# Kernel optimization log

Measured on AMD Instinct MI355X. Metric: run time of the kernel, lower is better.

## Reference

```python
import jax, jax.numpy as jnp
import numpy as np

B, F_DIM, FH, FW = 2, 2048, 64, 128
C, H, W = 19, 512, 1024


def resize_bilinear_ac(x, h, w):
    # align_corners=True bilinear resize of (B, C, H, W) -> (B, C, h, w)
    Bx, Cx, Hx, Wx = x.shape
    ys = jnp.linspace(0.0, Hx - 1.0, h)
    xs = jnp.linspace(0.0, Wx - 1.0, w)
    y0 = jnp.floor(ys).astype(jnp.int32)
    y1 = jnp.minimum(y0 + 1, Hx - 1)
    wy = (ys - y0).astype(x.dtype)
    x0 = jnp.floor(xs).astype(jnp.int32)
    x1 = jnp.minimum(x0 + 1, Wx - 1)
    wx = (xs - x0).astype(x.dtype)
    r = x[:, :, y0, :] * (1 - wy)[None, None, :, None] + x[:, :, y1, :] * wy[None, None, :, None]
    return r[:, :, :, x0] * (1 - wx) + r[:, :, :, x1] * wx


def setup_inputs() -> dict:
    key = jax.random.key(0)
    k1, k2, k3, k4 = jax.random.split(key, 4)
    return {
        "source_feat": jax.random.normal(k1, (B, F_DIM, FH, FW), dtype=jnp.float32),
        "source_softmax": jax.random.uniform(k2, (B, C, H, W), dtype=jnp.float32),
        "target_feat": jax.random.normal(k3, (B, F_DIM, FH, FW), dtype=jnp.float32),
        "target_softmax": jax.random.uniform(k4, (B, C, H, W), dtype=jnp.float32),
        "norm_order": 2,
    }


def _process(feat, softmax):
    # feat: (B, F, h, w) -> (B*h*w, F); labels from bilinear-downsampled softmax argmax
    h, w = feat.shape[2], feat.shape[3]
    f2 = feat.transpose(0, 2, 3, 1).reshape(-1, feat.shape[1])
    sm_dws = resize_bilinear_ac(softmax, h, w)
    labels = jnp.argmax(sm_dws, axis=1).reshape(-1)
    return f2, labels


def _forward(source_feat, source_softmax, target_feat, target_softmax, p):
    num_class = source_softmax.shape[1]
    fdim = source_feat.shape[1]
    sf, sl = _process(source_feat, source_softmax)
    tf, tl = _process(target_feat, target_softmax)

    # mixed centroids: per-class mean over concatenated source+target pixels
    sum_s = jax.ops.segment_sum(sf, sl, num_segments=num_class)
    cnt_s = jax.ops.segment_sum(jnp.ones(sf.shape[0], sf.dtype), sl, num_segments=num_class)
    sum_t = jax.ops.segment_sum(tf, tl, num_segments=num_class)
    cnt_t = jax.ops.segment_sum(jnp.ones(tf.shape[0], tf.dtype), tl, num_segments=num_class)
    cnt = cnt_s + cnt_t
    seen = cnt > 0
    centroids = (sum_s + sum_t) / jnp.maximum(cnt, 1.0)[:, None]  # (C, F)

    inv_p = 1.0 / p

    def f_dist(f2, lab, cnt_d):
        # torch: sum_i norm(centroid_i - feat_i, p) / (n_i * F) over classes with n_i>0, / count
        dp = jnp.sum(jnp.abs(f2 - centroids[lab]) ** p, axis=1)  # (N,)
        ssq = jax.ops.segment_sum(dp, lab, num_segments=num_class)  # (C,)
        valid = cnt_d > 0
        ssq_safe = jnp.where(valid, ssq, 1.0)
        per = ssq_safe ** inv_p / (jnp.maximum(cnt_d, 1.0) * fdim)
        return jnp.sum(jnp.where(valid, per, 0.0)) / jnp.sum(valid).astype(f2.dtype)

    f_dist_source = f_dist(sf, sl, cnt_s)
    f_dist_target = f_dist(tf, tl, cnt_t)

    # intra-domain centroid-to-centroid distance over seen classes
    n_seen = jnp.sum(seen).astype(centroids.dtype)
    diffp = jnp.sum(jnp.abs(centroids[:, None, :] - centroids[None, :, :]) ** p, axis=-1)  # (C, C)
    pair_mask = seen[:, None] & seen[None, :] & (~jnp.eye(num_class, dtype=bool))
    row = jnp.sum(jnp.where(pair_mask, diffp, 0.0), axis=1)
    row_safe = jnp.where(seen, row, 1.0)
    per_i = row_safe ** inv_p / ((n_seen - 1.0) * fdim)
    c_dist = jnp.sum(jnp.where(seen, per_i, 0.0)) / n_seen

    return jnp.stack([c_dist, f_dist_source, f_dist_target])


def reference(source_feat, source_softmax, target_feat, target_softmax, norm_order):
    return _forward(source_feat, source_softmax, target_feat, target_softmax, norm_order)
```

## Files before the change

### kernel.cpp

```cpp
#include <hip/hip_runtime.h>
#include <hip/hip_bf16.h>

#define BB 2
#define FDIM 2048
#define FH 64
#define FW 128
#define NPIX (FH*FW)
#define NC 19
#define SH 512
#define SW 1024

#define KS 4
#define PXS (NPIX/KS)

#define OFF_GCNT  0
#define OFF_SQP   38912
#define OFF_SUMP  194560
#define OFF_LAB   2684928
#define OFF_CENT  2717696
#define OFF_DOTSP 2873344
#define OFF_PQP   2875168
#define OFF_CNTF  2876384
#define OFF_ROW   2876536

typedef __attribute__((ext_vector_type(8))) short short8v;
typedef __attribute__((ext_vector_type(4))) float f32x4;
typedef __attribute__((ext_vector_type(4))) float f4v;

__device__ inline short f32_to_bf16_bits(float x) {
  __hip_bfloat16 h = __float2bfloat16(x);
  return *reinterpret_cast<short*>(&h);
}
__device__ inline float bf16_bits_to_f32(short s) {
  unsigned u = ((unsigned)s & 0xFFFFu) << 16;
  return __uint_as_float(u);
}

__global__ __launch_bounds__(256) void labels_kernel(
    const float* __restrict__ sm_s, const float* __restrict__ sm_t,
    unsigned char* __restrict__ labels, unsigned int* __restrict__ gcnt) {
  __shared__ float rowbuf[2][2][512];
  __shared__ unsigned int lcnt[NC];
  int tid = threadIdx.x;
  if (tid < NC) lcnt[tid] = 0u;

  int bid = blockIdx.x;
  int xh  = bid & 1;
  int oy  = (bid >> 1) & 63;
  int b   = (bid >> 7) & 1;
  int dom = bid >> 8;

  const float* sm = dom ? sm_t : sm_s;
  const float step_y = 511.0f / 63.0f;
  const float step_x = 1023.0f / 127.0f;
  float fy = __fmul_rn((float)oy, step_y);
  int y0 = (int)floorf(fy); int y1 = min(y0 + 1, SH - 1);
  float wy = __fsub_rn(fy, (float)y0);
  float omwy = __fsub_rn(1.0f, wy);

  int ox = xh * 64 + (tid & 63);
  float fx = __fmul_rn((float)ox, step_x);
  int x0 = (int)floorf(fx); int x1 = min(x0 + 1, SW - 1);
  float wx = __fsub_rn(fx, (float)x0);
  float omwx = __fsub_rn(1.0f, wx);
  int x0l = x0 - xh * 512, x1l = x1 - xh * 512;

  const float* base = sm + (size_t)b * (NC * SH * SW);
  int r   = tid >> 7;
  int col = (tid & 127) * 4;
  size_t choff = (size_t)(r ? y1 : y0) * SW + xh * 512 + col;

  f4v regs = *(const f4v*)(base + choff);
  *(f4v*)&rowbuf[0][r][col] = regs;

  float best = -1.0f; int bestc = 127;
  for (int c = 0; c < NC; ++c) {
    if (c < NC - 1)
      regs = *(const f4v*)(base + (size_t)(c + 1) * (SH * SW) + choff);
    __syncthreads();
    if (tid < 64) {
      float v00 = rowbuf[c & 1][0][x0l];
      float v01 = rowbuf[c & 1][0][x1l];
      float v10 = rowbuf[c & 1][1][x0l];
      float v11 = rowbuf[c & 1][1][x1l];
      float r0  = __fadd_rn(__fmul_rn(v00, omwy), __fmul_rn(v10, wy));
      float r1  = __fadd_rn(__fmul_rn(v01, omwy), __fmul_rn(v11, wy));
      float val = __fadd_rn(__fmul_rn(r0, omwx), __fmul_rn(r1, wx));
      if (val > best) { best = val; bestc = c; }
    }
    if (c < NC - 1)
      *(f4v*)&rowbuf[(c + 1) & 1][r][col] = regs;
  }
  if (tid < 64) {
    int pixid = dom * 16384 + b * 8192 + oy * 128 + ox;
    labels[pixid] = (unsigned char)bestc;
    atomicAdd(&lcnt[bestc], 1u);
  }
  __syncthreads();
  if (tid < NC) gcnt[bid * NC + tid] = lcnt[tid];
}

__global__ __launch_bounds__(256, 5) void segsum_kernel(
    const float* __restrict__ feat_s, const float* __restrict__ feat_t,
    const unsigned char* __restrict__ labels,
    float* __restrict__ sump, float* __restrict__ sq_p) {
  __shared__ unsigned short Abuf[4][16][128];

  int tid = threadIdx.x;
  int wv = tid >> 6, l = tid & 63;
  int m16 = l & 15, grp = l >> 4;
  int lhalf = l >> 5;
  int lpx   = (l & 31) * 4;

  int low = blockIdx.x & 255;
  int hi  = blockIdx.x >> 8;
  int d = low >> 7, strip = low & 127;
  int b = hi & 1, ks = hi >> 1;

  const float* feat = d ? feat_t : feat_s;
  int px0 = ks * PXS + wv * 512;
  const float* fbase = feat + ((size_t)(b * FDIM + strip * 16)) * NPIX + px0;
  const unsigned char* labp = labels + (d * 2 + b) * NPIX + px0;

  unsigned short (*mybuf)[128] = Abuf[wv];

  f32x4 accS0 = {0.f,0.f,0.f,0.f}, accS1 = {0.f,0.f,0.f,0.f};
  f32x4 accQ0 = {0.f,0.f,0.f,0.f}, accQ1 = {0.f,0.f,0.f,0.f};

  f4v ld[8];

#define LOADW(W)                                                              \
  _Pragma("unroll") for (int r = 0; r < 8; ++r)                               \
    ld[r] = *(const f4v*)(fbase + (size_t)(r * 2 + lhalf) * NPIX + (W) * 128 + lpx);

#define WRITEW()                                                              \
  _Pragma("unroll") for (int r = 0; r < 8; ++r) {                             \
    int row = r * 2 + lhalf;                                                  \
    unsigned u0 = ((unsigned)(unsigned short)f32_to_bf16_bits(ld[r].x)) |     \
                  (((unsigned)(unsigned short)f32_to_bf16_bits(ld[r].y)) << 16);\
    unsigned u1 = ((unsigned)(unsigned short)f32_to_bf16_bits(ld[r].z)) |     \
                  (((unsigned)(unsigned short)f32_to_bf16_bits(ld[r].w)) << 16);\
    int wbyte = (row * 256 + (l & 31) * 8) ^ ((row & 7) << 4);                \
    *(uint2*)((char*)&mybuf[0][0] + wbyte) = make_uint2(u0, u1);              \
  }

#define COMPW(W)                                                              \
  _Pragma("unroll") for (int kt = 0; kt < 4; ++kt) {                          \
    int rbyte = (m16 * 256 + kt * 64 + grp * 16) ^ ((m16 & 7) << 4);          \
    short8v a = *(const short8v*)((const char*)&mybuf[0][0] + rbyte);         \
    short8v a2;                                                               \
    _Pragma("unroll") for (int j = 0; j < 8; ++j) {                           \
      float x = bf16_bits_to_f32(a[j]);                                       \
      a2[j] = f32_to_bf16_bits(x * x);                                        \
    }                                                                         \
    uint2 lw = *(const uint2*)(labp + (W) * 128 + kt * 32 + grp * 8);         \
    short8v b0, b1;                                                           \
    _Pragma("unroll") for (int j = 0; j < 8; ++j) {                           \
      unsigned lab = ((j < 4 ? lw.x : lw.y) >> ((j & 3) * 8)) & 0xFFu;        \
      b0[j] = (lab == (unsigned)m16)        ? (short)0x3F80 : (short)0;       \
      b1[j] = (lab == (unsigned)(m16 + 16)) ? (short)0x3F80 : (short)0;       \
    }                                                                         \
    accS0 = __builtin_amdgcn_mfma_f32_16x16x32_bf16(a,  b0, accS0, 0, 0, 0);  \
    accS1 = __builtin_amdgcn_mfma_f32_16x16x32_bf16(a,  b1, accS1, 0, 0, 0);  \
    accQ0 = __builtin_amdgcn_mfma_f32_16x16x32_bf16(a2, b0, accQ0, 0, 0, 0);  \
    accQ1 = __builtin_amdgcn_mfma_f32_16x16x32_bf16(a2, b1, accQ1, 0, 0, 0);  \
  }

  LOADW(0);
  WRITEW();

#pragma unroll
  for (int w = 0; w < 4; ++w) {
    if (w < 3) { LOADW(w + 1); }
    COMPW(w);
    if (w < 3) { WRITEW(); }
  }
#undef LOADW
#undef WRITEW
#undef COMPW

  __syncthreads();
  float* Sred = (float*)&Abuf[0][0][0];
  float* Qred = Sred + 4 * 19 * 16;

  int c0 = l & 15, frb = (l >> 4) * 4;
  *(f32x4*)&Sred[(wv * 19 + c0) * 16 + frb] = accS0;
  if (c0 < 3) *(f32x4*)&Sred[(wv * 19 + 16 + c0) * 16 + frb] = accS1;

  float q0 = accQ0[0] + accQ0[1] + accQ0[2] + accQ0[3];
  float q1 = accQ1[0] + accQ1[1] + accQ1[2] + accQ1[3];
  q0 += __shfl_xor(q0, 16, 64); q0 += __shfl_xor(q0, 32, 64);
  q1 += __shfl_xor(q1, 16, 64); q1 += __shfl_xor(q1, 32, 64);
  if (l < 16) Qred[wv * 19 + l] = q0;
  if (l < 3)  Qred[wv * 19 + 16 + l] = q1;
  __syncthreads();

  float* myslice = sump + ((size_t)(hi * 2 + d) * NC) * FDIM + strip * 16;
  for (int t = tid; t < NC * 16; t += 256) {
    int c = t >> 4, fr = t & 15;
    float sv = Sred[(0 * 19 + c) * 16 + fr] + Sred[(1 * 19 + c) * 16 + fr] +
               Sred[(2 * 19 + c) * 16 + fr] + Sred[(3 * 19 + c) * 16 + fr];
    myslice[(size_t)c * FDIM + fr] = sv;
  }
  if (tid < NC) {
    float qv = Qred[tid] + Qred[19 + tid] + Qred[38 + tid] + Qred[57 + tid];
    sq_p[(size_t)((hi * 2 + d) * 128 + strip) * NC + tid] = qv;
  }
}

__device__ inline float block_reduce(float v, float* red, int tid) {
  red[tid] = v; __syncthreads();
  for (int s = 128; s > 0; s >>= 1) {
    if (tid < s) red[tid] += red[tid + s];
    __syncthreads();
  }
  float r = red[0];
  __syncthreads();
  return r;
}

__global__ __launch_bounds__(256) void centroid_kernel(
    const float* __restrict__ sump, const float* __restrict__ sq_p,
    const unsigned int* __restrict__ gcnt,
    float* __restrict__ cent, float* __restrict__ dotsp,
    float* __restrict__ pqp, float* __restrict__ cntf) {
  __shared__ float red[256];
  int bid = blockIdx.x;
  int c = bid % NC, j = bid / NC;
  int tid = threadIdx.x;

  float cs = block_reduce((float)gcnt[tid * NC + c], red, tid);
  float ct = block_reduce((float)gcnt[(256 + tid) * NC + c], red, tid);
  if (tid == 0 && j == 0) { cntf[c] = cs; cntf[NC + c] = ct; }
  float denom = fmaxf(cs + ct, 1.0f);

  int f = j * 256 + tid;
  float ssv = 0.f, stv = 0.f;
#pragma unroll
  for (int hi = 0; hi < 8; ++hi) {
    ssv += sump[((size_t)(hi * 2 + 0) * NC + c) * FDIM + f];
    stv += sump[((size_t)(hi * 2 + 1) * NC + c) * FDIM + f];
  }
  float cf = (ssv + stv) / denom;
  cent[(size_t)c * FDIM + f] = cf;

  float rds = block_reduce(cf * ssv, red, tid);
  float rdt = block_reduce(cf * stv, red, tid);
  float rcc = block_reduce(cf * cf, red, tid);

  int slice = tid >> 4, strip = j * 16 + (tid & 15);
  float v = sq_p[(size_t)(slice * 128 + strip) * NC + c];
  float qs = block_reduce((slice & 1) == 0 ? v : 0.f, red, tid);
  float qt = block_reduce((slice & 1) == 1 ? v : 0.f, red, tid);

  if (tid == 0) {
    dotsp[(j * NC + c) * 3 + 0] = rds;
    dotsp[(j * NC + c) * 3 + 1] = rdt;
    dotsp[(j * NC + c) * 3 + 2] = rcc;
    pqp[(j * NC + c) * 2 + 0] = qs;
    pqp[(j * NC + c) * 2 + 1] = qt;
  }
}

__global__ __launch_bounds__(256) void pair_kernel(
    const float* __restrict__ cent, const float* __restrict__ cntf,
    float* __restrict__ row) {
  __shared__ float red[256];
  int i = blockIdx.x;
  int tid = threadIdx.x;
  bool seen_i = (cntf[i] + cntf[NC + i]) > 0.f;
  float acc = 0.f;
  if (seen_i) {
    for (int j = 0; j < NC; ++j) {
      if (j == i) continue;
      if ((cntf[j] + cntf[NC + j]) <= 0.f) continue;
      for (int f = tid; f < FDIM; f += 256) {
        float dd = cent[(size_t)i * FDIM + f] - cent[(size_t)j * FDIM + f];
        acc += dd * dd;
      }
    }
  }
  float r = block_reduce(acc, red, tid);
  if (tid == 0) row[i] = r;
}

__global__ void final_kernel(
    const float* __restrict__ cntf, const float* __restrict__ dotsp,
    const float* __restrict__ pqp, const float* __restrict__ row,
    float* __restrict__ out) {
  int l = threadIdx.x;
  const float fdim = (float)FDIM;
  bool isC = l < NC;
  int c = isC ? l : 0;

  float cs = 0.f, ct = 0.f, qs = 0.f, qt = 0.f;
  float d_s = 0.f, d_t = 0.f, cc = 0.f, rw = 0.f;
  if (isC) {
    cs = cntf[c]; ct = cntf[NC + c];
#pragma unroll
    for (int j = 0; j < 8; ++j) {
      qs  += pqp[(j * NC + c) * 2 + 0];
      qt  += pqp[(j * NC + c) * 2 + 1];
      d_s += dotsp[(j * NC + c) * 3 + 0];
      d_t += dotsp[(j * NC + c) * 3 + 1];
      cc  += dotsp[(j * NC + c) * 3 + 2];
    }
    rw = row[c];
  }
  bool seen = isC && (cs + ct > 0.f);
  float nseenf = (float)__popcll(__ballot(seen));
  float nvs    = (float)__popcll(__ballot(isC && cs > 0.f));
  float nvt    = (float)__popcll(__ballot(isC && ct > 0.f));

  float fs = 0.f, ft = 0.f, cd = 0.f;
  if (isC && cs > 0.f) {
    float ssq = fmaxf(qs - 2.0f * d_s + cs * cc, 0.f);
    fs = sqrtf(ssq) / (cs * fdim);
  }
  if (isC && ct > 0.f) {
    float ssq = fmaxf(qt - 2.0f * d_t + ct * cc, 0.f);
    ft = sqrtf(ssq) / (ct * fdim);
  }
  if (seen) cd = sqrtf(rw) / ((nseenf - 1.0f) * fdim);

#pragma unroll
  for (int off = 32; off > 0; off >>= 1) {
    fs += __shfl_down(fs, off, 64);
    ft += __shfl_down(ft, off, 64);
    cd += __shfl_down(cd, off, 64);
  }
  if (l == 0) {
    out[0] = cd / nseenf;
    out[1] = fs / nvs;
    out[2] = ft / nvt;
  }
}

extern "C" void kernel_launch(void* const* d_in, const int* in_sizes, int n_in,
                              void* d_out, int out_size, void* d_ws, size_t ws_size,
                              hipStream_t stream) {
  const float* sfeat = (const float*)d_in[0];
  const float* ssm   = (const float*)d_in[1];
  const float* tfeat = (const float*)d_in[2];
  const float* tsm   = (const float*)d_in[3];
  float* out = (float*)d_out;

  char* ws = (char*)d_ws;
  unsigned int*  gcnt   = (unsigned int*)(ws + OFF_GCNT);
  float*         sq_p   = (float*)(ws + OFF_SQP);
  float*         sump   = (float*)(ws + OFF_SUMP);
  unsigned char* labels = (unsigned char*)(ws + OFF_LAB);
  float*         cent   = (float*)(ws + OFF_CENT);
  float*         dotsp  = (float*)(ws + OFF_DOTSP);
  float*         pqp    = (float*)(ws + OFF_PQP);
  float*         cntf   = (float*)(ws + OFF_CNTF);
  float*         row    = (float*)(ws + OFF_ROW);

  labels_kernel  <<<512,    256, 0, stream>>>(ssm, tsm, labels, gcnt);
  segsum_kernel  <<<2048,   256, 0, stream>>>(sfeat, tfeat, labels, sump, sq_p);
  centroid_kernel<<<NC * 8, 256, 0, stream>>>(sump, sq_p, gcnt, cent, dotsp, pqp, cntf);
  pair_kernel    <<<NC,     256, 0, stream>>>(cent, cntf, row);
  final_kernel   <<<1,      64,  0, stream>>>(cntf, dotsp, pqp, row, out);
}
```

Before: 106.5 us.

## Restructure segsum into 1024-thread blocks sharing a double-buffered LDS tile

The segment-sum kernel now uses 1024-thread blocks in which each of the 16 waves loads one feature row with wide contiguous loads. The tile goes into a block-shared, double-buffered LDS tile, and each wave computes the MFMA for its own 32-pixel k-slice. The pixel split drops from 4 to 2 chunks, which halves the partial-sum slices that the centroid kernel must reduce. In exchange the main loop now needs a block-wide barrier on every iteration, and per-thread work and in-flight loads shrink, which may reduce latency hiding.

```diff
diff --git a/kernel.cpp b/kernel.cpp
--- a/kernel.cpp
+++ b/kernel.cpp
@@ -10,7 +10,7 @@
 #define SH 512
 #define SW 1024
 
-#define KS 4
+#define KS 2
 #define PXS (NPIX/KS)
 
 #define OFF_GCNT  0
@@ -100,60 +100,62 @@
   if (tid < NC) gcnt[bid * NC + tid] = lcnt[tid];
 }
 
-__global__ __launch_bounds__(256, 5) void segsum_kernel(
+__global__ __launch_bounds__(1024, 8) void segsum_kernel(
     const float* __restrict__ feat_s, const float* __restrict__ feat_t,
     const unsigned char* __restrict__ labels,
     float* __restrict__ sump, float* __restrict__ sq_p) {
-  __shared__ unsigned short Abuf[4][16][128];
+  __shared__ unsigned short Abuf[2][16][512];
 
   int tid = threadIdx.x;
   int wv = tid >> 6, l = tid & 63;
   int m16 = l & 15, grp = l >> 4;
-  int lhalf = l >> 5;
-  int lpx   = (l & 31) * 4;
-
-  int low = blockIdx.x & 255;
-  int hi  = blockIdx.x >> 8;
-  int d = low >> 7, strip = low & 127;
-  int b = hi & 1, ks = hi >> 1;
+
+  int bid = blockIdx.x;
+  int strip = bid & 127;
+  int d  = (bid >> 7) & 1;
+  int b  = (bid >> 8) & 1;
+  int ks = bid >> 9;
+  int hi = ks * 2 + b;
 
   const float* feat = d ? feat_t : feat_s;
-  int px0 = ks * PXS + wv * 512;
-  const float* fbase = feat + ((size_t)(b * FDIM + strip * 16)) * NPIX + px0;
-  const unsigned char* labp = labels + (d * 2 + b) * NPIX + px0;
-
-  unsigned short (*mybuf)[128] = Abuf[wv];
+  const float* myrow = feat + ((size_t)(b * FDIM + strip * 16 + wv)) * NPIX + ks * PXS;
+  const unsigned char* labp = labels + (d * 2 + b) * NPIX + ks * PXS;
 
   f32x4 accS0 = {0.f,0.f,0.f,0.f}, accS1 = {0.f,0.f,0.f,0.f};
   f32x4 accQ0 = {0.f,0.f,0.f,0.f}, accQ1 = {0.f,0.f,0.f,0.f};
 
-  f4v ld[8];
+  f4v ld0, ld1;
 
 #define LOADW(W)                                                              \
-  _Pragma("unroll") for (int r = 0; r < 8; ++r)                               \
-    ld[r] = *(const f4v*)(fbase + (size_t)(r * 2 + lhalf) * NPIX + (W) * 128 + lpx);
-
-#define WRITEW()                                                              \
-  _Pragma("unroll") for (int r = 0; r < 8; ++r) {                             \
-    int row = r * 2 + lhalf;                                                  \
-    unsigned u0 = ((unsigned)(unsigned short)f32_to_bf16_bits(ld[r].x)) |     \
-                  (((unsigned)(unsigned short)f32_to_bf16_bits(ld[r].y)) << 16);\
-    unsigned u1 = ((unsigned)(unsigned short)f32_to_bf16_bits(ld[r].z)) |     \
-                  (((unsigned)(unsigned short)f32_to_bf16_bits(ld[r].w)) << 16);\
-    int wbyte = (row * 256 + (l & 31) * 8) ^ ((row & 7) << 4);                \
-    *(uint2*)((char*)&mybuf[0][0] + wbyte) = make_uint2(u0, u1);              \
-  }
-
-#define COMPW(W)                                                              \
-  _Pragma("unroll") for (int kt = 0; kt < 4; ++kt) {                          \
-    int rbyte = (m16 * 256 + kt * 64 + grp * 16) ^ ((m16 & 7) << 4);          \
-    short8v a = *(const short8v*)((const char*)&mybuf[0][0] + rbyte);         \
+  ld0 = *(const f4v*)(myrow + (W) * 512 + l * 4);                             \
+  ld1 = *(const f4v*)(myrow + (W) * 512 + 256 + l * 4);
+
+#define WRITEW(BUF)                                                           \
+  {                                                                           \
+    unsigned u0 = ((unsigned)(unsigned short)f32_to_bf16_bits(ld0.x)) |       \
+                  (((unsigned)(unsigned short)f32_to_bf16_bits(ld0.y)) << 16);\
+    unsigned u1 = ((unsigned)(unsigned short)f32_to_bf16_bits(ld0.z)) |       \
+                  (((unsigned)(unsigned short)f32_to_bf16_bits(ld0.w)) << 16);\
+    unsigned u2 = ((unsigned)(unsigned short)f32_to_bf16_bits(ld1.x)) |       \
+                  (((unsigned)(unsigned short)f32_to_bf16_bits(ld1.y)) << 16);\
+    unsigned u3 = ((unsigned)(unsigned short)f32_to_bf16_bits(ld1.z)) |       \
+                  (((unsigned)(unsigned short)f32_to_bf16_bits(ld1.w)) << 16);\
+    int wb0 = (wv * 1024 + l * 8) ^ ((wv & 7) << 4);                          \
+    int wb1 = (wv * 1024 + 512 + l * 8) ^ ((wv & 7) << 4);                    \
+    *(uint2*)((char*)&Abuf[BUF][0][0] + wb0) = make_uint2(u0, u1);            \
+    *(uint2*)((char*)&Abuf[BUF][0][0] + wb1) = make_uint2(u2, u3);            \
+  }
+
+#define COMPW(W, BUF)                                                         \
+  {                                                                           \
+    int rbyte = (m16 * 1024 + wv * 64 + grp * 16) ^ ((m16 & 7) << 4);         \
+    short8v a = *(const short8v*)((const char*)&Abuf[BUF][0][0] + rbyte);     \
     short8v a2;                                                               \
     _Pragma("unroll") for (int j = 0; j < 8; ++j) {                           \
       float x = bf16_bits_to_f32(a[j]);                                       \
       a2[j] = f32_to_bf16_bits(x * x);                                        \
     }                                                                         \
-    uint2 lw = *(const uint2*)(labp + (W) * 128 + kt * 32 + grp * 8);         \
+    uint2 lw = *(const uint2*)(labp + (W) * 512 + wv * 32 + grp * 8);         \
     short8v b0, b1;                                                           \
     _Pragma("unroll") for (int j = 0; j < 8; ++j) {                           \
       unsigned lab = ((j < 4 ? lw.x : lw.y) >> ((j & 3) * 8)) & 0xFFu;        \
@@ -167,13 +169,18 @@
   }
 
   LOADW(0);
-  WRITEW();
-
-#pragma unroll
-  for (int w = 0; w < 4; ++w) {
-    if (w < 3) { LOADW(w + 1); }
-    COMPW(w);
-    if (w < 3) { WRITEW(); }
+  WRITEW(0);
+  LOADW(1);
+  __syncthreads();
+
+#pragma unroll
+  for (int w = 0; w < 8; ++w) {
+    COMPW(w, w & 1);
+    if (w < 7) {
+      WRITEW((w + 1) & 1);
+      if (w < 6) { LOADW(w + 2); }
+    }
+    __syncthreads();
   }
 #undef LOADW
 #undef WRITEW
@@ -181,7 +188,7 @@
 
   __syncthreads();
   float* Sred = (float*)&Abuf[0][0][0];
-  float* Qred = Sred + 4 * 19 * 16;
+  float* Qred = Sred + 16 * 19 * 16;
 
   int c0 = l & 15, frb = (l >> 4) * 4;
   *(f32x4*)&Sred[(wv * 19 + c0) * 16 + frb] = accS0;
@@ -196,15 +203,19 @@
   __syncthreads();
 
   float* myslice = sump + ((size_t)(hi * 2 + d) * NC) * FDIM + strip * 16;
-  for (int t = tid; t < NC * 16; t += 256) {
-    int c = t >> 4, fr = t & 15;
-    float sv = Sred[(0 * 19 + c) * 16 + fr] + Sred[(1 * 19 + c) * 16 + fr] +
-               Sred[(2 * 19 + c) * 16 + fr] + Sred[(3 * 19 + c) * 16 + fr];
+  if (tid < NC * 16) {
+    int c = tid >> 4, fr = tid & 15;
+    float sv = 0.f;
+#pragma unroll
+    for (int v = 0; v < 16; ++v) sv += Sred[(v * 19 + c) * 16 + fr];
     myslice[(size_t)c * FDIM + fr] = sv;
   }
-  if (tid < NC) {
-    float qv = Qred[tid] + Qred[19 + tid] + Qred[38 + tid] + Qred[57 + tid];
-    sq_p[(size_t)((hi * 2 + d) * 128 + strip) * NC + tid] = qv;
+  if (tid >= 512 && tid < 512 + NC) {
+    int c = tid - 512;
+    float qv = 0.f;
+#pragma unroll
+    for (int v = 0; v < 16; ++v) qv += Qred[v * 19 + c];
+    sq_p[(size_t)((hi * 2 + d) * 128 + strip) * NC + c] = qv;
   }
 }
 
@@ -237,7 +248,7 @@
   int f = j * 256 + tid;
   float ssv = 0.f, stv = 0.f;
 #pragma unroll
-  for (int hi = 0; hi < 8; ++hi) {
+  for (int hi = 0; hi < 4; ++hi) {
     ssv += sump[((size_t)(hi * 2 + 0) * NC + c) * FDIM + f];
     stv += sump[((size_t)(hi * 2 + 1) * NC + c) * FDIM + f];
   }
@@ -249,9 +260,9 @@
   float rcc = block_reduce(cf * cf, red, tid);
 
   int slice = tid >> 4, strip = j * 16 + (tid & 15);
-  float v = sq_p[(size_t)(slice * 128 + strip) * NC + c];
-  float qs = block_reduce((slice & 1) == 0 ? v : 0.f, red, tid);
-  float qt = block_reduce((slice & 1) == 1 ? v : 0.f, red, tid);
+  float v = (tid < 128) ? sq_p[(size_t)(slice * 128 + strip) * NC + c] : 0.f;
+  float qs = block_reduce((tid < 128 && (slice & 1) == 0) ? v : 0.f, red, tid);
+  float qt = block_reduce((tid < 128 && (slice & 1) == 1) ? v : 0.f, red, tid);
 
   if (tid == 0) {
     dotsp[(j * NC + c) * 3 + 0] = rds;
@@ -356,9 +367,9 @@
   float*         cntf   = (float*)(ws + OFF_CNTF);
   float*         row    = (float*)(ws + OFF_ROW);
 
-  labels_kernel  <<<512,    256, 0, stream>>>(ssm, tsm, labels, gcnt);
-  segsum_kernel  <<<2048,   256, 0, stream>>>(sfeat, tfeat, labels, sump, sq_p);
-  centroid_kernel<<<NC * 8, 256, 0, stream>>>(sump, sq_p, gcnt, cent, dotsp, pqp, cntf);
-  pair_kernel    <<<NC,     256, 0, stream>>>(cent, cntf, row);
-  final_kernel   <<<1,      64,  0, stream>>>(cntf, dotsp, pqp, row, out);
-}
+  labels_kernel  <<<512,    256,  0, stream>>>(ssm, tsm, labels, gcnt);
+  segsum_kernel  <<<1024,   1024, 0, stream>>>(sfeat, tfeat, labels, sump, sq_p);
+  centroid_kernel<<<NC * 8, 256,  0, stream>>>(sump, sq_p, gcnt, cent, dotsp, pqp, cntf);
+  pair_kernel    <<<NC,     256,  0, stream>>>(cent, cntf, row);
+  final_kernel   <<<1,      64,   0, stream>>>(cntf, dotsp, pqp, row, out);
+}
```

New measurement: 110.7 us. 1.04x slower.
